# Kernel tuning notes

Measured on AMD Instinct MI355X. Metric: run time of the kernel, lower is better.

Reference implementation:

```python
import jax, jax.numpy as jnp
import numpy as np

NUM_LONGTERM_MEM = 16  # config.num_longterm_mem


def setup_inputs() -> dict:
    key = jax.random.key(0)
    ks = jax.random.split(key, 9)
    B, T, C, H = 32, 2048, 768, 1536
    s = 0.02
    return {
        "x": jax.random.normal(ks[0], (B, T, C), jnp.float32),
        "Wq": jax.random.normal(ks[1], (C, C), jnp.float32) * s,
        "bq": jax.random.normal(ks[2], (C,), jnp.float32) * s,
        "W0": jax.random.normal(ks[3], (B, H, C), jnp.float32) * s,
        "b0": jax.random.normal(ks[4], (B, H), jnp.float32) * s,
        "W1": jax.random.normal(ks[5], (B, C, H), jnp.float32) * s,
        "b1": jax.random.normal(ks[6], (B, C), jnp.float32) * s,
        "Wo": jax.random.normal(ks[7], (C, C), jnp.float32) * s,
        "bo": jax.random.normal(ks[8], (C,), jnp.float32) * s,
    }


def reference(x, Wq, bq, W0, b0, W1, b1, Wo, bo):
    # x: [B, T, C]. Per-sample memory MLP weights W0 [B,H,C], W1 [B,C,H].
    B, T, C = x.shape
    L = NUM_LONGTERM_MEM
    # query projection (nn.Linear: x @ W^T + b)
    q = jnp.einsum("btc,dc->btd", x, Wq) + bq                       # [B,T,C]
    # per-sample 2-layer memory MLP with SiLU
    h = jax.nn.silu(jnp.einsum("btc,bhc->bth", q, W0) + b0[:, None, :])  # [B,T,H]
    mem = jnp.einsum("bth,bch->btc", h, W1) + b1[:, None, :]        # [B,T,C]
    # adaptive_avg_pool1d over T -> L (T divisible by L => uniform window mean)
    pooled = mem.reshape(B, L, T // L, C).mean(axis=2)              # [B,L,C]
    # output projection
    return jnp.einsum("blc,dc->bld", pooled, Wo) + bo               # [B,L,C]
```

## Files before the change

### kernel.cpp

```cpp
#include <hip/hip_runtime.h>
#include <stdint.h>

#define B_ 32
#define T_ 2048
#define C_ 768
#define H_ 1536
#define L_ 16

typedef unsigned short u16;
typedef __bf16 bf16x8 __attribute__((ext_vector_type(8)));
typedef float f32x4 __attribute__((ext_vector_type(4)));

__device__ __forceinline__ u16 f2bf(float f) {
    union { float f; uint32_t u; } v; v.f = f;
    uint32_t r = (v.u + 0x7fffu + ((v.u >> 16) & 1u)) >> 16;
    return (u16)r;
}

__device__ __forceinline__ float wave_sum(float v) {
    v += __shfl_xor(v, 1);  v += __shfl_xor(v, 2);  v += __shfl_xor(v, 4);
    v += __shfl_xor(v, 8);  v += __shfl_xor(v, 16); v += __shfl_xor(v, 32);
    return v;
}

__global__ void k_cvt(const float* __restrict__ in, u16* __restrict__ out, int n4) {
    int stride = gridDim.x * blockDim.x;
    for (int i = blockIdx.x * blockDim.x + threadIdx.x; i < n4; i += stride) {
        float4 v = reinterpret_cast<const float4*>(in)[i];
        ushort4 o;
        o.x = f2bf(v.x); o.y = f2bf(v.y); o.z = f2bf(v.z); o.w = f2bf(v.w);
        reinterpret_cast<ushort4*>(out)[i] = o;
    }
}

__device__ __forceinline__ void stage_bf16_gload(const u16* gtile, int ld, u16* Ts,
                                                 int w, int lane) {
    const int r_in = lane >> 3;
    const int c0   = (lane & 7) << 3;
#pragma unroll
    for (int j = 0; j < 4; ++j) {
        int row = ((w << 2) + j) * 8 + r_in;
        const u16* g = gtile + (size_t)row * ld + c0;
        u16* l = Ts + (((w << 2) + j) << 9);
        __builtin_amdgcn_global_load_lds((const __attribute__((address_space(1))) void*)g,
                                         (__attribute__((address_space(3))) void*)l,
                                         16, 0, 0);
    }
}

__device__ __forceinline__ void stage_f32_cvt(const float* gtile, int ld, u16* Ts, int t) {
#pragma unroll
    for (int i = 0; i < 8; ++i) {
        int slot = t + (i << 8);
        int row  = slot >> 4;
        int c4   = (slot & 15) << 2;
        float4 v = *reinterpret_cast<const float4*>(gtile + (size_t)row * ld + c4);
        ushort4 o;
        o.x = f2bf(v.x); o.y = f2bf(v.y); o.z = f2bf(v.z); o.w = f2bf(v.w);
        *reinterpret_cast<ushort4*>(&Ts[row * 64 + c4]) = o;
    }
}

__device__ __forceinline__ void mfma_tile(const u16* As, const u16* Bs,
                                          f32x4 (&acc)[4][4], int wr, int wc, int lane) {
#pragma unroll
    for (int ks = 0; ks < 2; ++ks) {
        const int ko = (ks << 5) + ((lane >> 4) << 3);
        bf16x8 a[4], b[4];
#pragma unroll
        for (int m = 0; m < 4; ++m)
            a[m] = *reinterpret_cast<const bf16x8*>(&As[(wr * 64 + m * 16 + (lane & 15)) * 64 + ko]);
#pragma unroll
        for (int n = 0; n < 4; ++n)
            b[n] = *reinterpret_cast<const bf16x8*>(&Bs[(wc * 64 + n * 16 + (lane & 15)) * 64 + ko]);
#pragma unroll
        for (int m = 0; m < 4; ++m)
#pragma unroll
            for (int n = 0; n < 4; ++n)
                acc[m][n] = __builtin_amdgcn_mfma_f32_16x16x32_bf16(a[m], b[n], acc[m][n], 0, 0, 0);
    }
}

__global__ __launch_bounds__(256, 2) void k_gemm1(const float* __restrict__ x,
                                                  const u16* __restrict__ Wqb,
                                                  const float* __restrict__ bq,
                                                  u16* __restrict__ qb) {
    __shared__ u16 As[128 * 64];
    __shared__ u16 Bs[128 * 64];
    const int t = threadIdx.x, w = t >> 6, lane = t & 63;
    const int wr = w >> 1, wc = w & 1;
    const int m0 = blockIdx.y * 128;
    const int n0 = blockIdx.x * 128;

    f32x4 acc[4][4];
#pragma unroll
    for (int m = 0; m < 4; ++m)
#pragma unroll
        for (int n = 0; n < 4; ++n) acc[m][n] = (f32x4){0.f, 0.f, 0.f, 0.f};

    for (int kt = 0; kt < C_ / 64; ++kt) {
        stage_f32_cvt(x + (size_t)m0 * C_ + kt * 64, C_, As, t);
        stage_bf16_gload(Wqb + (size_t)n0 * C_ + kt * 64, C_, Bs, w, lane);
        __syncthreads();
        mfma_tile(As, Bs, acc, wr, wc, lane);
        __syncthreads();
    }

    const int r0 = m0 + wr * 64 + ((lane >> 4) << 2);
    const int cb = n0 + wc * 64 + (lane & 15);
#pragma unroll
    for (int n = 0; n < 4; ++n) {
        int c = cb + n * 16;
        float bb = bq[c];
#pragma unroll
        for (int m = 0; m < 4; ++m)
#pragma unroll
            for (int r = 0; r < 4; ++r) {
                int row = r0 + m * 16 + r;
                qb[(size_t)row * C_ + c] = f2bf(acc[m][n][r] + bb);
            }
    }
}

template <bool BPRE>
__global__ __launch_bounds__(256, 2) void k_gemm2(const u16* __restrict__ qb,
                                                  const u16* __restrict__ W0b,
                                                  const float* __restrict__ W0f,
                                                  const float* __restrict__ b0,
                                                  float* __restrict__ ph) {
    __shared__ u16 As[128 * 64];
    __shared__ u16 Bs[128 * 64];
    __shared__ float Ps[2][128];
    const int t = threadIdx.x, w = t >> 6, lane = t & 63;
    const int wr = w >> 1, wc = w & 1;
    const int b  = blockIdx.z;
    const int mt = blockIdx.y;
    const int n0 = blockIdx.x * 128;
    const u16* Abase = qb + ((size_t)b * T_ + mt * 128) * C_;

    f32x4 acc[4][4];
#pragma unroll
    for (int m = 0; m < 4; ++m)
#pragma unroll
        for (int n = 0; n < 4; ++n) acc[m][n] = (f32x4){0.f, 0.f, 0.f, 0.f};

    for (int kt = 0; kt < C_ / 64; ++kt) {
        stage_bf16_gload(Abase + kt * 64, C_, As, w, lane);
        if (BPRE)
            stage_bf16_gload(W0b + ((size_t)b * H_ + n0) * C_ + kt * 64, C_, Bs, w, lane);
        else
            stage_f32_cvt(W0f + ((size_t)b * H_ + n0) * C_ + kt * 64, C_, Bs, t);
        __syncthreads();
        mfma_tile(As, Bs, acc, wr, wc, lane);
        __syncthreads();
    }

    float s[4];
#pragma unroll
    for (int n = 0; n < 4; ++n) {
        int c = n0 + wc * 64 + n * 16 + (lane & 15);
        float bb = b0[b * H_ + c];
        float sum = 0.f;
#pragma unroll
        for (int m = 0; m < 4; ++m)
#pragma unroll
            for (int r = 0; r < 4; ++r) {
                float v = acc[m][n][r] + bb;
                v = v / (1.f + __expf(-v));
                sum += v;
            }
        sum += __shfl_xor(sum, 16);
        sum += __shfl_xor(sum, 32);
        s[n] = sum;
    }
    if (lane < 16) {
#pragma unroll
        for (int n = 0; n < 4; ++n) Ps[wr][wc * 64 + n * 16 + lane] = s[n];
    }
    __syncthreads();
    if (t < 128) {
        float v = (Ps[0][t] + Ps[1][t]) * (1.f / 128.f);
        ph[((size_t)b * L_ + mt) * H_ + n0 + t] = v;
    }
}

__global__ __launch_bounds__(256) void k_3a(const float* __restrict__ ph,
                                            const float* __restrict__ W1,
                                            const float* __restrict__ b1,
                                            float* __restrict__ pooled) {
    const int t = threadIdx.x, w = t >> 6, lane = t & 63;
    const int b  = blockIdx.y;
    const int cb = blockIdx.x * 16 + w * 4;

    float acc[4][16];
#pragma unroll
    for (int g = 0; g < 4; ++g)
#pragma unroll
        for (int l = 0; l < 16; ++l) acc[g][l] = 0.f;

    for (int i = 0; i < H_ / 256; ++i) {
        int h0 = i * 256 + lane * 4;
        float4 wv[4];
#pragma unroll
        for (int g = 0; g < 4; ++g)
            wv[g] = *reinterpret_cast<const float4*>(W1 + ((size_t)b * C_ + cb + g) * H_ + h0);
#pragma unroll
        for (int l = 0; l < 16; ++l) {
            float4 pv = *reinterpret_cast<const float4*>(ph + ((size_t)b * L_ + l) * H_ + h0);
#pragma unroll
            for (int g = 0; g < 4; ++g)
                acc[g][l] += wv[g].x * pv.x + wv[g].y * pv.y + wv[g].z * pv.z + wv[g].w * pv.w;
        }
    }
#pragma unroll
    for (int g = 0; g < 4; ++g)
#pragma unroll
        for (int l = 0; l < 16; ++l) acc[g][l] = wave_sum(acc[g][l]);

    if (lane < 16) {
#pragma unroll
        for (int g = 0; g < 4; ++g)
            pooled[((size_t)b * L_ + lane) * C_ + cb + g] = acc[g][lane] + b1[b * C_ + cb + g];
    }
}

__global__ __launch_bounds__(256) void k_3b(const float* __restrict__ pooled,
                                            const float* __restrict__ Wo,
                                            const float* __restrict__ bo,
                                            float* __restrict__ out) {
    __shared__ __align__(16) float ps[4 * 768];
    const int t = threadIdx.x, w = t >> 6, lane = t & 63;
    const int rr0 = blockIdx.x * 4;

    for (int idx = t; idx < 4 * 768; idx += 256)
        ps[idx] = pooled[(size_t)rr0 * 768 + idx];
    __syncthreads();

    for (int d = w; d < 768; d += 4) {
        float a0 = 0.f, a1 = 0.f, a2 = 0.f, a3 = 0.f;
#pragma unroll
        for (int i = 0; i < 3; ++i) {
            int c = i * 256 + lane * 4;
            float4 wv = *reinterpret_cast<const float4*>(Wo + (size_t)d * 768 + c);
            float4 p0 = *reinterpret_cast<const float4*>(&ps[0 * 768 + c]);
            float4 p1 = *reinterpret_cast<const float4*>(&ps[1 * 768 + c]);
            float4 p2 = *reinterpret_cast<const float4*>(&ps[2 * 768 + c]);
            float4 p3 = *reinterpret_cast<const float4*>(&ps[3 * 768 + c]);
            a0 += wv.x * p0.x + wv.y * p0.y + wv.z * p0.z + wv.w * p0.w;
            a1 += wv.x * p1.x + wv.y * p1.y + wv.z * p1.z + wv.w * p1.w;
            a2 += wv.x * p2.x + wv.y * p2.y + wv.z * p2.z + wv.w * p2.w;
            a3 += wv.x * p3.x + wv.y * p3.y + wv.z * p3.z + wv.w * p3.w;
        }
        a0 = wave_sum(a0); a1 = wave_sum(a1); a2 = wave_sum(a2); a3 = wave_sum(a3);
        if (lane == 0) {
            float bb = bo[d];
            out[(size_t)(rr0 + 0) * 768 + d] = a0 + bb;
            out[(size_t)(rr0 + 1) * 768 + d] = a1 + bb;
            out[(size_t)(rr0 + 2) * 768 + d] = a2 + bb;
            out[(size_t)(rr0 + 3) * 768 + d] = a3 + bb;
        }
    }
}

extern "C" void kernel_launch(void* const* d_in, const int* in_sizes, int n_in,
                              void* d_out, int out_size, void* d_ws, size_t ws_size,
                              hipStream_t stream) {
    const float* x  = (const float*)d_in[0];
    const float* Wq = (const float*)d_in[1];
    const float* bq = (const float*)d_in[2];
    const float* W0 = (const float*)d_in[3];
    const float* b0 = (const float*)d_in[4];
    const float* W1 = (const float*)d_in[5];
    const float* b1 = (const float*)d_in[6];
    const float* Wo = (const float*)d_in[7];
    const float* bo = (const float*)d_in[8];
    float* out = (float*)d_out;

    char* p = (char*)d_ws;
    size_t off = 0;
    auto carve = [&](size_t bytes) -> char* {
        char* r = p + off;
        off += (bytes + 255) & ~(size_t)255;
        return r;
    };
    u16*   qb     = (u16*)carve((size_t)B_ * T_ * C_ * 2);
    u16*   Wqb    = (u16*)carve((size_t)C_ * C_ * 2);
    float* ph     = (float*)carve((size_t)B_ * L_ * H_ * 4);
    float* pooled = (float*)carve((size_t)B_ * L_ * C_ * 4);
    size_t w0b_bytes = (size_t)B_ * H_ * C_ * 2;
    u16* W0b = nullptr;
    if (off + w0b_bytes <= ws_size) W0b = (u16*)carve(w0b_bytes);

    k_cvt<<<dim3(64), 256, 0, stream>>>(Wq, Wqb, C_ * C_ / 4);
    if (W0b)
        k_cvt<<<dim3(2048), 256, 0, stream>>>(W0, W0b, B_ * H_ * C_ / 4);

    k_gemm1<<<dim3(C_ / 128, (B_ * T_) / 128), 256, 0, stream>>>(x, Wqb, bq, qb);

    if (W0b)
        k_gemm2<true><<<dim3(H_ / 128, L_, B_), 256, 0, stream>>>(qb, W0b, nullptr, b0, ph);
    else
        k_gemm2<false><<<dim3(H_ / 128, L_, B_), 256, 0, stream>>>(qb, nullptr, W0, b0, ph);

    k_3a<<<dim3(C_ / 16, B_), 256, 0, stream>>>(ph, W1, b1, pooled);
    k_3b<<<dim3(B_ * L_ / 4), 256, 0, stream>>>(pooled, Wo, bo, out);
}
```

Baseline: 713.8 us.

## Add 256x256 double-buffered MFMA GEMM kernel with pre-converted bf16 inputs

Measured after the change: 667.1 us. 1.07x faster.

```diff
diff --git a/kernel.cpp b/kernel.cpp
--- a/kernel.cpp
+++ b/kernel.cpp
@@ -33,6 +33,173 @@
     }
 }
 
+__device__ __forceinline__ void gload16(const u16* g, u16* l) {
+    __builtin_amdgcn_global_load_lds((const __attribute__((address_space(1))) void*)g,
+                                     (__attribute__((address_space(3))) void*)l, 16, 0, 0);
+}
+
+#define PH_SYNC() do { __builtin_amdgcn_s_barrier(); \
+    asm volatile("s_waitcnt lgkmcnt(0)" ::: "memory"); \
+    __builtin_amdgcn_sched_barrier(0); } while (0)
+#define PH_END() do { __builtin_amdgcn_sched_barrier(0); __builtin_amdgcn_s_barrier(); } while (0)
+
+template <int EPI>
+__global__ __launch_bounds__(512, 2) void k_gemm8(const u16* __restrict__ Aall,
+                                                  const u16* __restrict__ Ball,
+                                                  const float* __restrict__ biasall,
+                                                  u16* __restrict__ qout,
+                                                  float* __restrict__ ph) {
+    __shared__ u16 sm[65536];
+    const int t = threadIdx.x;
+    const int w = t >> 6, lane = t & 63;
+    const int wr = w >> 2, wc = w & 3;
+    const int l15 = lane & 15, kq = lane >> 4, cx = lane & 7;
+
+    const int n0 = blockIdx.x * 256;
+    const int m0 = blockIdx.y * 256;
+    const u16* A; const u16* Bm; const float* bias;
+    if constexpr (EPI == 0) {
+        A = Aall + (size_t)m0 * C_;
+        Bm = Ball + (size_t)n0 * C_;
+        bias = biasall + n0;
+    } else {
+        const int b = blockIdx.z;
+        A = Aall + ((size_t)b * T_ + m0) * C_;
+        Bm = Ball + ((size_t)b * H_ + n0) * C_;
+        bias = biasall + (size_t)b * H_ + n0;
+    }
+
+    const int rl = (w << 4) + (lane >> 3);
+    const int cs = (((lane & 7) ^ ((lane >> 3) & 7)) << 3);
+    const int ldst = (w << 10);
+
+    auto stA = [&](int kt, int h) {
+        const u16* g = A + (size_t)(h * 128 + rl) * C_ + kt * 64 + cs;
+        u16* l = sm + (kt & 1) * 32768 + h * 8192 + ldst;
+        gload16(g, l);
+        gload16(g + 8 * C_, l + 512);
+    };
+    auto stB = [&](int kt, int h) {
+        const u16* g = Bm + (size_t)(h * 128 + rl) * C_ + kt * 64 + cs;
+        u16* l = sm + (kt & 1) * 32768 + 16384 + h * 8192 + ldst;
+        gload16(g, l);
+        gload16(g + 8 * C_, l + 512);
+    };
+
+    f32x4 acc[8][4];
+#pragma unroll
+    for (int m = 0; m < 8; ++m)
+#pragma unroll
+        for (int n = 0; n < 4; ++n) acc[m][n] = (f32x4){0.f, 0.f, 0.f, 0.f};
+
+    bf16x8 a0[4][2], a1[4][2], bfr[2][2];
+
+    auto rdA = [&](bf16x8 (&a)[4][2], int bt, int mq) {
+        const u16* Ah = sm + bt * 32768 + wr * 8192;
+#pragma unroll
+        for (int mm = 0; mm < 4; ++mm) {
+            const u16* rp = Ah + ((mq * 4 + mm) * 16 + l15) * 64;
+#pragma unroll
+            for (int ks = 0; ks < 2; ++ks)
+                a[mm][ks] = *reinterpret_cast<const bf16x8*>(rp + ((((ks << 2) + kq) ^ cx) << 3));
+        }
+    };
+    auto rdB = [&](int bt, int qn) {
+        const u16* Bh = sm + bt * 32768 + 16384 + (wc >> 1) * 8192;
+        const int cb = (wc & 1) * 64 + qn * 32;
+#pragma unroll
+        for (int nn = 0; nn < 2; ++nn) {
+            const u16* cp = Bh + (cb + nn * 16 + l15) * 64;
+#pragma unroll
+            for (int ks = 0; ks < 2; ++ks)
+                bfr[nn][ks] = *reinterpret_cast<const bf16x8*>(cp + ((((ks << 2) + kq) ^ cx) << 3));
+        }
+    };
+    auto mma16 = [&](bf16x8 (&a)[4][2], int mq, int qn) {
+        __builtin_amdgcn_s_setprio(1);
+#pragma unroll
+        for (int ks = 0; ks < 2; ++ks)
+#pragma unroll
+            for (int mm = 0; mm < 4; ++mm)
+#pragma unroll
+                for (int nn = 0; nn < 2; ++nn)
+                    acc[mq * 4 + mm][qn * 2 + nn] = __builtin_amdgcn_mfma_f32_16x16x32_bf16(
+                        a[mm][ks], bfr[nn][ks], acc[mq * 4 + mm][qn * 2 + nn], 0, 0, 0);
+        __builtin_amdgcn_s_setprio(0);
+    };
+
+    stA(0, 0); stA(0, 1); stB(0, 0); stB(0, 1);
+    stA(1, 0); stA(1, 1);
+    asm volatile("s_waitcnt vmcnt(4)" ::: "memory");
+    __builtin_amdgcn_s_barrier();
+
+#pragma unroll 1
+    for (int kt = 0; kt < 12; ++kt) {
+        const int bt = kt & 1;
+        rdA(a0, bt, 0);
+        rdB(bt, 0);
+        if (kt + 1 < 12) stB(kt + 1, 0);
+        PH_SYNC();
+        mma16(a0, 0, 0);
+        PH_END();
+        rdA(a1, bt, 1);
+        if (kt + 1 < 12) stB(kt + 1, 1);
+        PH_SYNC();
+        mma16(a1, 1, 0);
+        PH_END();
+        rdB(bt, 1);
+        if (kt + 2 < 12) stA(kt + 2, 0);
+        PH_SYNC();
+        mma16(a0, 0, 1);
+        PH_END();
+        if (kt + 2 < 12) {
+            stA(kt + 2, 1);
+            asm volatile("s_waitcnt vmcnt(4)" ::: "memory");
+        } else {
+            asm volatile("s_waitcnt vmcnt(0)" ::: "memory");
+        }
+        __builtin_amdgcn_s_barrier();
+        __builtin_amdgcn_sched_barrier(0);
+        mma16(a1, 1, 1);
+        PH_END();
+    }
+
+    if constexpr (EPI == 0) {
+        const int colb = n0 + wc * 64 + l15;
+        const int rowb = m0 + wr * 128 + (kq << 2);
+#pragma unroll
+        for (int n = 0; n < 4; ++n) {
+            float bv = bias[wc * 64 + n * 16 + l15];
+            int c = colb + n * 16;
+#pragma unroll
+            for (int m = 0; m < 8; ++m)
+#pragma unroll
+                for (int r = 0; r < 4; ++r)
+                    qout[(size_t)(rowb + m * 16 + r) * C_ + c] = f2bf(acc[m][n][r] + bv);
+        }
+    } else {
+        const int b = blockIdx.z;
+        const int lwin = blockIdx.y * 2 + wr;
+#pragma unroll
+        for (int n = 0; n < 4; ++n) {
+            int cloc = wc * 64 + n * 16 + l15;
+            float bv = bias[cloc];
+            float s = 0.f;
+#pragma unroll
+            for (int m = 0; m < 8; ++m)
+#pragma unroll
+                for (int r = 0; r < 4; ++r) {
+                    float v = acc[m][n][r] + bv;
+                    s += v / (1.f + __expf(-v));
+                }
+            s += __shfl_xor(s, 16);
+            s += __shfl_xor(s, 32);
+            if (kq == 0)
+                ph[((size_t)b * L_ + lwin) * H_ + n0 + cloc] = s * (1.f / 128.f);
+        }
+    }
+}
+
 __device__ __forceinline__ void stage_bf16_gload(const u16* gtile, int ld, u16* Ts,
                                                  int w, int lane) {
     const int r_in = lane >> 3;
@@ -42,9 +209,7 @@
         int row = ((w << 2) + j) * 8 + r_in;
         const u16* g = gtile + (size_t)row * ld + c0;
         u16* l = Ts + (((w << 2) + j) << 9);
-        __builtin_amdgcn_global_load_lds((const __attribute__((address_space(1))) void*)g,
-                                         (__attribute__((address_space(3))) void*)l,
-                                         16, 0, 0);
+        gload16(g, l);
     }
 }
 
@@ -115,10 +280,8 @@
 #pragma unroll
         for (int m = 0; m < 4; ++m)
 #pragma unroll
-            for (int r = 0; r < 4; ++r) {
-                int row = r0 + m * 16 + r;
-                qb[(size_t)row * C_ + c] = f2bf(acc[m][n][r] + bb);
-            }
+            for (int r = 0; r < 4; ++r)
+                qb[(size_t)(r0 + m * 16 + r) * C_ + c] = f2bf(acc[m][n][r] + bb);
     }
 }
 
@@ -166,8 +329,7 @@
 #pragma unroll
             for (int r = 0; r < 4; ++r) {
                 float v = acc[m][n][r] + bb;
-                v = v / (1.f + __expf(-v));
-                sum += v;
+                sum += v / (1.f + __expf(-v));
             }
         sum += __shfl_xor(sum, 16);
         sum += __shfl_xor(sum, 32);
@@ -178,10 +340,8 @@
         for (int n = 0; n < 4; ++n) Ps[wr][wc * 64 + n * 16 + lane] = s[n];
     }
     __syncthreads();
-    if (t < 128) {
-        float v = (Ps[0][t] + Ps[1][t]) * (1.f / 128.f);
-        ph[((size_t)b * L_ + mt) * H_ + n0 + t] = v;
-    }
+    if (t < 128)
+        ph[((size_t)b * L_ + mt) * H_ + n0 + t] = (Ps[0][t] + Ps[1][t]) * (1.f / 128.f);
 }
 
 __global__ __launch_bounds__(256) void k_3a(const float* __restrict__ ph,
@@ -287,20 +447,32 @@
     u16*   Wqb    = (u16*)carve((size_t)C_ * C_ * 2);
     float* ph     = (float*)carve((size_t)B_ * L_ * H_ * 4);
     float* pooled = (float*)carve((size_t)B_ * L_ * C_ * 4);
-    size_t w0b_bytes = (size_t)B_ * H_ * C_ * 2;
-    u16* W0b = nullptr;
-    if (off + w0b_bytes <= ws_size) W0b = (u16*)carve(w0b_bytes);
-
-    k_cvt<<<dim3(64), 256, 0, stream>>>(Wq, Wqb, C_ * C_ / 4);
-    if (W0b)
+
+    const size_t xb_bytes  = (size_t)B_ * T_ * C_ * 2;
+    const size_t w0b_bytes = (size_t)B_ * H_ * C_ * 2;
+
+    if (off + xb_bytes <= ws_size) {
+        u16* xb  = (u16*)carve(xb_bytes);
+        u16* W0b = xb;
+
+        k_cvt<<<dim3(2048), 256, 0, stream>>>(x, xb, B_ * T_ * C_ / 4);
+        k_cvt<<<dim3(64), 256, 0, stream>>>(Wq, Wqb, C_ * C_ / 4);
+        k_gemm8<0><<<dim3(C_ / 256, (B_ * T_) / 256), 512, 0, stream>>>(xb, Wqb, bq, qb, nullptr);
         k_cvt<<<dim3(2048), 256, 0, stream>>>(W0, W0b, B_ * H_ * C_ / 4);
-
-    k_gemm1<<<dim3(C_ / 128, (B_ * T_) / 128), 256, 0, stream>>>(x, Wqb, bq, qb);
-
-    if (W0b)
-        k_gemm2<true><<<dim3(H_ / 128, L_, B_), 256, 0, stream>>>(qb, W0b, nullptr, b0, ph);
-    else
-        k_gemm2<false><<<dim3(H_ / 128, L_, B_), 256, 0, stream>>>(qb, nullptr, W0, b0, ph);
+        k_gemm8<1><<<dim3(H_ / 256, T_ / 256, B_), 512, 0, stream>>>(qb, W0b, b0, nullptr, ph);
+    } else {
+        u16* W0b = nullptr;
+        if (off + w0b_bytes <= ws_size) W0b = (u16*)carve(w0b_bytes);
+
+        k_cvt<<<dim3(64), 256, 0, stream>>>(Wq, Wqb, C_ * C_ / 4);
+        if (W0b)
+            k_cvt<<<dim3(2048), 256, 0, stream>>>(W0, W0b, B_ * H_ * C_ / 4);
+        k_gemm1<<<dim3(C_ / 128, (B_ * T_) / 128), 256, 0, stream>>>(x, Wqb, bq, qb);
+        if (W0b)
+            k_gemm2<true><<<dim3(H_ / 128, L_, B_), 256, 0, stream>>>(qb, W0b, nullptr, b0, ph);
+        else
+            k_gemm2<false><<<dim3(H_ / 128, L_, B_), 256, 0, stream>>>(qb, nullptr, W0, b0, ph);
+    }
 
     k_3a<<<dim3(C_ / 16, B_), 256, 0, stream>>>(ph, W1, b1, pooled);
     k_3b<<<dim3(B_ * L_ / 4), 256, 0, stream>>>(pooled, Wo, bo, out);
```
